# Optimization experiments

Measured on AMD Instinct MI355X. Metric: run time of the kernel, lower is better.

The kernel has to match this reference:

```python
import jax, jax.numpy as jnp
import numpy as np

B, C, H, W = 2, 64, 96, 96
C8 = C // 8

def _conv1x1(x, w, b):
    # x: [B, Cin, H, W], w: [Cout, Cin], b: [Cout]
    return jnp.einsum('oi,bihw->bohw', w, x) + b[None, :, None, None]

def setup_inputs() -> dict:
    key = jax.random.key(0)
    ks = jax.random.split(key, 10)
    s = lambda fan_in: 1.0 / np.sqrt(fan_in)
    return {
        'feature_maps': jax.random.normal(ks[0], (B, C, H, W), jnp.float32),
        'depth': jax.random.normal(ks[1], (B, 1, H, W), jnp.float32),
        'wa': jax.random.normal(ks[2], (C, 1), jnp.float32) * s(1),
        'ba': jax.random.normal(ks[3], (C,), jnp.float32) * s(1),
        'wb': jax.random.normal(ks[4], (C8, C), jnp.float32) * s(C),
        'bb': jax.random.normal(ks[5], (C8,), jnp.float32) * s(C),
        'wc': jax.random.normal(ks[6], (C8, C), jnp.float32) * s(C),
        'bc': jax.random.normal(ks[7], (C8,), jnp.float32) * s(C),
        'wd': jax.random.normal(ks[8], (C, C), jnp.float32) * s(C),
        'bd': jax.random.normal(ks[9], (C,), jnp.float32) * s(C),
    }

def reference(feature_maps, depth, wa, ba, wb, bb, wc, bc, wd, bd):
    b, c, h, w = feature_maps.shape
    n = h * w
    depth_feat = jax.nn.relu(_conv1x1(depth, wa, ba))          # [B,C,H,W]
    feat_b = _conv1x1(feature_maps, wb, bb).reshape(b, -1, n)  # [B,C/8,N]
    feat_b = jnp.transpose(feat_b, (0, 2, 1))                  # [B,N,C/8]
    feat_c = _conv1x1(depth_feat, wc, bc).reshape(b, -1, n)    # [B,C/8,N]
    attn = jax.nn.softmax(jnp.einsum('bnk,bkm->bnm', feat_b, feat_c), axis=-1)  # [B,N,N]
    feat_d = _conv1x1(depth_feat, wd, bd).reshape(b, -1, n)    # [B,C,N]
    # bmm(feat_d, attn^T): out[b,c,n] = sum_m feat_d[b,c,m] * attn[b,n,m]
    feat_e = jnp.einsum('bcm,bnm->bcn', feat_d, attn)
    return feat_e.reshape(b, c, h, w)
```

## Files before the change

### kernel.cpp

```cpp
#include <hip/hip_runtime.h>


#define BN 2
#define CC 64
#define C8K 8
#define NN 9216
#define MCHUNK 128
#define TQ 128
#define NBLKQ (NN / TQ)
#define PREP_PX 64
#define LOG2E 1.44269504f
#define PSTR 132

typedef __attribute__((ext_vector_type(8))) short short8;
typedef __attribute__((ext_vector_type(16))) float f32x16;

#define OFF_QB 0
#define OFF_KT (OFF_QB + BN * NN * C8K / 2)
#define OFF_VT (OFF_KT + BN * NN * C8K / 2)
#define OFF_PACC (OFF_VT + BN * NN * CC / 2)

static __device__ inline unsigned f2bf(float x) {
    unsigned u = __builtin_bit_cast(unsigned, x);
    return (u + 0x7fff + ((u >> 16) & 1)) >> 16;
}

#if __has_builtin(__builtin_amdgcn_cvt_pk_bf16_f32)
typedef __attribute__((ext_vector_type(2))) __bf16 bf16x2;
static __device__ inline unsigned pk_pair(float lo, float hi) {
    bf16x2 v = __builtin_amdgcn_cvt_pk_bf16_f32(lo, hi);
    return __builtin_bit_cast(unsigned, v);
}
#else
static __device__ inline unsigned pk_pair(float lo, float hi) {
    unsigned ulo = __builtin_bit_cast(unsigned, lo) + 0x8000u;
    unsigned uhi = __builtin_bit_cast(unsigned, hi) + 0x8000u;
    return __builtin_amdgcn_perm(uhi, ulo, 0x07060302u);
}
#endif

__global__ __launch_bounds__(256) void pam_prep(
    const float* __restrict__ fm, const float* __restrict__ depth,
    const float* __restrict__ wa, const float* __restrict__ ba,
    const float* __restrict__ wb, const float* __restrict__ bb,
    const float* __restrict__ wc, const float* __restrict__ bc,
    const float* __restrict__ wd, const float* __restrict__ bd,
    unsigned short* __restrict__ Qb, unsigned short* __restrict__ Kt,
    unsigned short* __restrict__ Vt)
{
    __shared__ float s_wd[CC * CC];
    __shared__ float s_wb[C8K * CC], s_wc[C8K * CC];
    __shared__ float s_wa[CC], s_ba[CC], s_bd[CC];
    __shared__ float s_bb[C8K], s_bc[C8K];
    __shared__ float qp[4][PREP_PX][C8K + 1];

    int t = threadIdx.x;
    for (int i = t; i < CC * CC; i += 256) s_wd[i] = wd[i];
    for (int i = t; i < C8K * CC; i += 256) { s_wb[i] = wb[i]; s_wc[i] = wc[i]; }
    if (t < CC) { s_wa[t] = wa[t]; s_ba[t] = ba[t]; s_bd[t] = bd[t]; }
    if (t < C8K) { s_bb[t] = bb[t]; s_bc[t] = bc[t]; }
    __syncthreads();

    int px0 = blockIdx.x * PREP_PX;
    int b = px0 / NN;
    int m0 = px0 - b * NN;
    int px = t & 63, w = t >> 6;
    int m = m0 + px;
    int gidx = px0 + px;

    float d = depth[gidx];
    float df[CC];
#pragma unroll
    for (int i = 0; i < CC; ++i) df[i] = fmaxf(s_wa[i] * d + s_ba[i], 0.0f);

#pragma unroll 4
    for (int cc = 0; cc < 16; ++cc) {
        int c = w * 16 + cc;
        float acc = s_bd[c];
#pragma unroll
        for (int i = 0; i < CC; i += 4) {
            float4 wv = *(const float4*)&s_wd[c * CC + i];
            acc += wv.x * df[i] + wv.y * df[i + 1] + wv.z * df[i + 2] + wv.w * df[i + 3];
        }
        Vt[(b * CC + c) * NN + m] = (unsigned short)f2bf(acc);
    }

    {
        float k0 = s_bc[2 * w], k1 = s_bc[2 * w + 1];
#pragma unroll
        for (int i = 0; i < CC; ++i) {
            k0 += s_wc[(2 * w) * CC + i] * df[i];
            k1 += s_wc[(2 * w + 1) * CC + i] * df[i];
        }
        unsigned pkv = f2bf(k0) | (f2bf(k1) << 16);
        *(unsigned*)&Kt[(b * NN + m) * C8K + 2 * w] = pkv;
    }

    {
        float q[C8K];
#pragma unroll
        for (int k = 0; k < C8K; ++k) q[k] = (w == 0) ? s_bb[k] : 0.0f;
#pragma unroll
        for (int ii = 0; ii < 16; ++ii) {
            int i = w * 16 + ii;
            float f = fm[(b * CC + i) * NN + m];
#pragma unroll
            for (int k = 0; k < C8K; ++k) q[k] += s_wb[k * CC + i] * f;
        }
#pragma unroll
        for (int k = 0; k < C8K; ++k) qp[w][px][k] = q[k];
    }
    __syncthreads();
    {
        int px2 = t >> 2, k2 = (t & 3) * 2;
        float a0 = (qp[0][px2][k2] + qp[1][px2][k2] + qp[2][px2][k2] + qp[3][px2][k2]) * LOG2E;
        float a1 = (qp[0][px2][k2 + 1] + qp[1][px2][k2 + 1] + qp[2][px2][k2 + 1] + qp[3][px2][k2 + 1]) * LOG2E;
        unsigned pkv = f2bf(a0) | (f2bf(a1) << 16);
        *(unsigned*)&Qb[(px0 + px2) * C8K + k2] = pkv;
    }
}

__global__ __launch_bounds__(256, 4) void pam_attn(
    const unsigned short* __restrict__ Qb, const unsigned short* __restrict__ Kt,
    const unsigned short* __restrict__ Vt,
    unsigned short* __restrict__ PACC, float* __restrict__ PSUM,
    int m_range)
{
    __shared__ unsigned short v_s[CC * PSTR];

    int t = threadIdx.x;
    int n0 = blockIdx.x * TQ;
    int split = blockIdx.y;
    int b = blockIdx.z;
    int m_start = split * m_range;
    int nchunk = m_range / MCHUNK;

    int lane = t & 63, w = t >> 6;
    int l31 = lane & 31, half = lane >> 5;

    short8 bq = {};
    if (lane < 32) bq = *(const short8*)&Qb[(b * NN + n0 + w * 32 + l31) * C8K];
    else           bq[0] = (short)f2bf(-12.0f * LOG2E);

    const unsigned mand = half ? 0xFFFF0000u : 0xFFFFFFFFu;
    const unsigned mor  = half ? 0x00003F80u : 0u;

    f32x16 acc0 = {}, acc1 = {};
    float2 rs2 = {0.0f, 0.0f};

    const unsigned short* vr0 = &v_s[l31 * PSTR + half * 4];
    const unsigned short* vr1 = &v_s[(32 + l31) * PSTR + half * 4];

    int vrow = t >> 2, vsl = t & 3;

    for (int ch = 0; ch < nchunk; ++ch) {
        int m0 = m_start + ch * MCHUNK;
        ulonglong2 vbuf[4];
        {
            const unsigned short* gsrc = &Vt[(b * CC + vrow) * NN + m0 + vsl * 8];
#pragma unroll
            for (int i = 0; i < 4; ++i)
                vbuf[i] = *(const ulonglong2*)(gsrc + i * 32);
        }
        union { unsigned u[4]; short8 s8; } aK[4];
#pragma unroll
        for (int mt = 0; mt < 4; ++mt)
            aK[mt].s8 = *(const short8*)&Kt[(b * NN + m0 + mt * 32 + l31) * C8K];
#pragma unroll
        for (int mt = 0; mt < 4; ++mt)
            aK[mt].u[0] = (aK[mt].u[0] & mand) | mor;

        __syncthreads();
        {
            unsigned long long* ldst =
                (unsigned long long*)&v_s[vrow * PSTR + vsl * 8];
#pragma unroll
            for (int i = 0; i < 4; ++i) {
                ldst[i * 8 + 0] = vbuf[i].x;
                ldst[i * 8 + 1] = vbuf[i].y;
            }
        }
        __syncthreads();

#pragma unroll
        for (int mt = 0; mt < 4; ++mt) {
            f32x16 s = __builtin_amdgcn_mfma_f32_32x32x16_bf16(aK[mt].s8, bq, (f32x16){}, 0, 0, 0);
            unsigned qd[8];
#pragma unroll
            for (int i = 0; i < 8; ++i) {
                float e0 = __builtin_amdgcn_exp2f(s[2 * i]);
                float e1 = __builtin_amdgcn_exp2f(s[2 * i + 1]);
                rs2.x += e0; rs2.y += e1;
                qd[i] = pk_pair(e0, e1);
            }
#pragma unroll
            for (int ks = 0; ks < 2; ++ks) {
                union { unsigned u[4]; short8 s8; } Bp;
#pragma unroll
                for (int i = 0; i < 4; ++i) Bp.u[i] = qd[ks * 4 + i];
                const int off = mt * 32 + ks * 16;
                union { unsigned long long d[2]; short8 s8; } A0, A1;
                A0.d[0] = *(const unsigned long long*)(vr0 + off);
                A0.d[1] = *(const unsigned long long*)(vr0 + off + 8);
                A1.d[0] = *(const unsigned long long*)(vr1 + off);
                A1.d[1] = *(const unsigned long long*)(vr1 + off + 8);
                acc0 = __builtin_amdgcn_mfma_f32_32x32x16_bf16(A0.s8, Bp.s8, acc0, 0, 0, 0);
                acc1 = __builtin_amdgcn_mfma_f32_32x32x16_bf16(A1.s8, Bp.s8, acc1, 0, 0, 0);
            }
        }
    }

    float rsum = rs2.x + rs2.y;
    rsum += __shfl_xor(rsum, 32);
    if (lane < 32)
        PSUM[(split * BN + b) * NN + n0 + w * 32 + l31] = rsum;

    {
        int slabc = (split * BN + b) * CC;
        int nidx = n0 + w * 32 + l31;
#pragma unroll
        for (int reg = 0; reg < 16; ++reg) {
            int c = 8 * (reg >> 2) + (reg & 3) + 4 * half;
            PACC[(slabc + c) * NN + nidx] = (unsigned short)f2bf(acc0[reg]);
            PACC[(slabc + 32 + c) * NN + nidx] = (unsigned short)f2bf(acc1[reg]);
        }
    }
}

__global__ __launch_bounds__(256) void pam_norm(
    const unsigned short* __restrict__ PACC, const float* __restrict__ PSUM,
    float* __restrict__ out, int S)
{
    __shared__ float s_inv[64];
    int t = threadIdx.x;
    int n0 = blockIdx.x * 64;
    int b = blockIdx.y;
    if (t < 64) {
        float s = 0.0f;
        for (int sp = 0; sp < S; ++sp) s += PSUM[(sp * BN + b) * NN + n0 + t];
        s_inv[t] = 1.0f / s;
    }
    __syncthreads();

    int c = t >> 2, ng = t & 3;
    int nb = n0 + ng * 16;
    float a[16];
#pragma unroll
    for (int j = 0; j < 16; ++j) a[j] = 0.0f;

    for (int sp = 0; sp < S; ++sp) {
        const unsigned short* p = &PACC[((sp * BN + b) * CC + c) * NN + nb];
        uint4 u0 = *(const uint4*)p;
        uint4 u1 = *(const uint4*)(p + 8);
        const unsigned uu[8] = {u0.x, u0.y, u0.z, u0.w, u1.x, u1.y, u1.z, u1.w};
#pragma unroll
        for (int i = 0; i < 8; ++i) {
            a[2 * i]     += __builtin_bit_cast(float, uu[i] << 16);
            a[2 * i + 1] += __builtin_bit_cast(float, uu[i] & 0xffff0000u);
        }
    }
    float* o = &out[(b * CC + c) * NN + nb];
#pragma unroll
    for (int j4 = 0; j4 < 4; ++j4) {
        float4 v;
        v.x = a[j4 * 4 + 0] * s_inv[ng * 16 + j4 * 4 + 0];
        v.y = a[j4 * 4 + 1] * s_inv[ng * 16 + j4 * 4 + 1];
        v.z = a[j4 * 4 + 2] * s_inv[ng * 16 + j4 * 4 + 2];
        v.w = a[j4 * 4 + 3] * s_inv[ng * 16 + j4 * 4 + 3];
        *(float4*)(o + j4 * 4) = v;
    }
}

extern "C" void kernel_launch(void* const* d_in, const int* in_sizes, int n_in,
                              void* d_out, int out_size, void* d_ws, size_t ws_size,
                              hipStream_t stream) {
    const float* fm    = (const float*)d_in[0];
    const float* depth = (const float*)d_in[1];
    const float* wa    = (const float*)d_in[2];
    const float* ba    = (const float*)d_in[3];
    const float* wb    = (const float*)d_in[4];
    const float* bb    = (const float*)d_in[5];
    const float* wc    = (const float*)d_in[6];
    const float* bc    = (const float*)d_in[7];
    const float* wd    = (const float*)d_in[8];
    const float* bd    = (const float*)d_in[9];
    float* out = (float*)d_out;

    float* ws = (float*)d_ws;
    unsigned short* Qb = (unsigned short*)(ws + OFF_QB);
    unsigned short* Kt = (unsigned short*)(ws + OFF_KT);
    unsigned short* Vt = (unsigned short*)(ws + OFF_VT);
    unsigned short* PACC = (unsigned short*)(ws + OFF_PACC);

    int S = 12;
    while (S > 4) {
        size_t need = (size_t)OFF_PACC * 4
                    + (size_t)S * BN * NN * CC * 2
                    + (size_t)S * BN * NN * 4;
        if (need <= ws_size) break;
        S -= 4;
    }
    float* PSUM = (float*)(PACC + (size_t)S * BN * NN * CC);
    int m_range = NN / S;

    pam_prep<<<dim3((BN * NN) / PREP_PX), 256, 0, stream>>>(
        fm, depth, wa, ba, wb, bb, wc, bc, wd, bd, Qb, Kt, Vt);
    pam_attn<<<dim3(NBLKQ, S, BN), 256, 0, stream>>>(Qb, Kt, Vt, PACC, PSUM, m_range);
    pam_norm<<<dim3(NN / 64, BN), 256, 0, stream>>>(PACC, PSUM, out, S);
}
```

Baseline: 141.5 us.

## Give each wave a private V tile to remove block-wide barriers

```diff
diff --git a/kernel.cpp b/kernel.cpp
--- a/kernel.cpp
+++ b/kernel.cpp
@@ -5,12 +5,12 @@
 #define CC 64
 #define C8K 8
 #define NN 9216
-#define MCHUNK 128
+#define MCHUNK 64
 #define TQ 128
 #define NBLKQ (NN / TQ)
 #define PREP_PX 64
 #define LOG2E 1.44269504f
-#define PSTR 132
+#define VSTR 68
 
 typedef __attribute__((ext_vector_type(8))) short short8;
 typedef __attribute__((ext_vector_type(16))) float f32x16;
@@ -126,7 +126,7 @@
     unsigned short* __restrict__ PACC, float* __restrict__ PSUM,
     int m_range)
 {
-    __shared__ unsigned short v_s[CC * PSTR];
+    __shared__ unsigned short v_s[4][64 * VSTR];
 
     int t = threadIdx.x;
     int n0 = blockIdx.x * TQ;
@@ -148,42 +148,48 @@
     f32x16 acc0 = {}, acc1 = {};
     float2 rs2 = {0.0f, 0.0f};
 
-    const unsigned short* vr0 = &v_s[l31 * PSTR + half * 4];
-    const unsigned short* vr1 = &v_s[(32 + l31) * PSTR + half * 4];
-
-    int vrow = t >> 2, vsl = t & 3;
+    unsigned short* vq = v_s[w];
+    const unsigned short* vr0 = vq + l31 * VSTR + half * 4;
+    const unsigned short* vr1 = vq + (32 + l31) * VSTR + half * 4;
+
+    int srow = lane >> 2;
+    int sseg = lane & 3;
 
     for (int ch = 0; ch < nchunk; ++ch) {
         int m0 = m_start + ch * MCHUNK;
-        ulonglong2 vbuf[4];
-        {
-            const unsigned short* gsrc = &Vt[(b * CC + vrow) * NN + m0 + vsl * 8];
-#pragma unroll
-            for (int i = 0; i < 4; ++i)
-                vbuf[i] = *(const ulonglong2*)(gsrc + i * 32);
-        }
-        union { unsigned u[4]; short8 s8; } aK[4];
-#pragma unroll
-        for (int mt = 0; mt < 4; ++mt)
+
+        union { unsigned u[4]; short8 s8; } aK[2];
+#pragma unroll
+        for (int mt = 0; mt < 2; ++mt)
             aK[mt].s8 = *(const short8*)&Kt[(b * NN + m0 + mt * 32 + l31) * C8K];
 #pragma unroll
-        for (int mt = 0; mt < 4; ++mt)
+        for (int mt = 0; mt < 2; ++mt)
             aK[mt].u[0] = (aK[mt].u[0] & mand) | mor;
 
-        __syncthreads();
-        {
-            unsigned long long* ldst =
-                (unsigned long long*)&v_s[vrow * PSTR + vsl * 8];
-#pragma unroll
-            for (int i = 0; i < 4; ++i) {
-                ldst[i * 8 + 0] = vbuf[i].x;
-                ldst[i * 8 + 1] = vbuf[i].y;
+#pragma unroll
+        for (int pb = 0; pb < 2; ++pb) {
+            ulonglong2 vb[4];
+#pragma unroll
+            for (int p = 0; p < 2; ++p) {
+                int r = (pb * 2 + p) * 16 + srow;
+                const unsigned short* g = &Vt[(b * CC + r) * NN + m0 + sseg * 16];
+                vb[p * 2 + 0] = *(const ulonglong2*)(g);
+                vb[p * 2 + 1] = *(const ulonglong2*)(g + 8);
             }
-        }
-        __syncthreads();
-
-#pragma unroll
-        for (int mt = 0; mt < 4; ++mt) {
+#pragma unroll
+            for (int p = 0; p < 2; ++p) {
+                int r = (pb * 2 + p) * 16 + srow;
+                unsigned long long* d =
+                    (unsigned long long*)(vq + r * VSTR + sseg * 16);
+                d[0] = vb[p * 2 + 0].x;
+                d[1] = vb[p * 2 + 0].y;
+                d[2] = vb[p * 2 + 1].x;
+                d[3] = vb[p * 2 + 1].y;
+            }
+        }
+
+#pragma unroll
+        for (int mt = 0; mt < 2; ++mt) {
             f32x16 s = __builtin_amdgcn_mfma_f32_32x32x16_bf16(aK[mt].s8, bq, (f32x16){}, 0, 0, 0);
             unsigned qd[8];
 #pragma unroll
```

After: 148.2 us. 1.05x slower.
